# Optimization experiments

Hardware: AMD Instinct MI355X
Metric: run time of the kernel (lower is better)

## Reference

```python
import jax, jax.numpy as jnp
import numpy as np
from functools import partial

TAU = 2.0
BN_EPS = 1e-5
SG_ALPHA = 4.0  # spikingjelly surrogate.Sigmoid default

@jax.custom_vjp
def heaviside(x):
    return (x >= 0.0).astype(x.dtype)

def _heaviside_fwd(x):
    return heaviside(x), x

def _heaviside_bwd(x, g):
    s = jax.nn.sigmoid(SG_ALPHA * x)
    return (g * SG_ALPHA * s * (1.0 - s),)

heaviside.defvjp(_heaviside_fwd, _heaviside_bwd)

def lif(x_seq, v_threshold=1.0):
    # MultiStepLIFNode: tau=2, decay_input=True, v_reset=0 (hard reset), detach_reset
    def step(v, x):
        v = v + (x - v) / TAU
        s = heaviside(v - v_threshold)
        v = v * (1.0 - jax.lax.stop_gradient(s))
        return v, s
    _, s_seq = jax.lax.scan(step, jnp.zeros_like(x_seq[0]), x_seq)
    return s_seq

def conv1x1_bn(x, w, gamma, beta, mean, var, b=None):
    # x: [T,B,C,N]; w: [Cout,Cin]; 1x1 conv == channel matmul; BN in eval mode
    y = jnp.einsum('oc,tbcn->tbon', w, x)
    if b is not None:
        y = y + b[:, None]
    inv = gamma / jnp.sqrt(var + BN_EPS)
    return y * inv[:, None] + (beta - mean * inv)[:, None]

def setup_inputs() -> dict:
    key = jax.random.key(0)
    ks = jax.random.split(key, 24)
    T, B, C, N = 4, 32, 384, 196
    d = {}
    d['x'] = jax.random.normal(ks[0], (T, B, C, N), dtype=jnp.float32)
    d['policy'] = jax.random.uniform(ks[1], (T * B, N, 1), dtype=jnp.float32)
    scale = 1.0 / np.sqrt(C)
    for i, p in enumerate(['q', 'k', 'v', 'proj']):
        base = 2 + i * 5
        d[p + '_w'] = jax.random.normal(ks[base], (C, C), dtype=jnp.float32) * scale
        d[p + '_gamma'] = jnp.ones((C,), jnp.float32)
        d[p + '_beta'] = jnp.zeros((C,), jnp.float32)
        d[p + '_mean'] = jax.random.normal(ks[base + 1], (C,), dtype=jnp.float32) * 0.1
        d[p + '_var'] = jax.random.uniform(ks[base + 2], (C,), dtype=jnp.float32, minval=0.5, maxval=1.5)
    d['proj_b'] = jnp.zeros((C,), jnp.float32)
    return d

def _to_heads(s, H):
    T, B, C, N = s.shape
    # [T,B,C,N] -> [T,B,N,H,D] -> [T,B,H,N,D]
    return s.transpose(0, 1, 3, 2).reshape(T, B, N, H, C // H).transpose(0, 1, 3, 2, 4)

def reference(x, policy, q_w, q_gamma, q_beta, q_mean, q_var,
              k_w, k_gamma, k_beta, k_mean, k_var,
              v_w, v_gamma, v_beta, v_mean, v_var,
              proj_w, proj_gamma, proj_beta, proj_mean, proj_var, proj_b):
    T, B, C, N = x.shape
    H = 12
    attn_scale = 0.25
    q = _to_heads(lif(conv1x1_bn(x, q_w, q_gamma, q_beta, q_mean, q_var)), H)
    k = _to_heads(lif(conv1x1_bn(x, k_w, k_gamma, k_beta, k_mean, k_var)), H)
    v = _to_heads(lif(conv1x1_bn(x, v_w, v_gamma, v_beta, v_mean, v_var)), H)
    attn = jnp.einsum('tbhnd,tbhmd->tbhnm', q, k)
    # attention_policy: attn *= (policy + (1-policy)*eye)
    pol = policy.reshape(T, B, 1, 1, N)
    eye = jnp.eye(N, dtype=attn.dtype)
    attn = attn * (pol + (1.0 - pol) * eye)
    y = jnp.einsum('tbhnm,tbhmd->tbhnd', attn, v) * attn_scale
    y = y.transpose(0, 1, 2, 4, 3).reshape(T, B, C, N)
    y = lif(y, v_threshold=0.5)
    y = conv1x1_bn(y, proj_w, proj_gamma, proj_beta, proj_mean, proj_var, b=proj_b)
    return lif(y)
```

## Files before the change

kernel.cpp:

```cpp
#include <hip/hip_runtime.h>

typedef unsigned int u32;
typedef __bf16 bf16x8 __attribute__((ext_vector_type(8)));
typedef __bf16 bf16x4v __attribute__((ext_vector_type(4)));
typedef _Float16 f16x8 __attribute__((ext_vector_type(8)));
typedef float f32x4 __attribute__((ext_vector_type(4)));

#define Tn 4
#define Bn 32
#define Cn 384
#define Nn 196
#define Hn 12
#define CNn (Cn*Nn)
#define BCNn (Bn*CNn)
#define BHNn (Bn*Hn*Nn)
#define PBITS (Tn*BHNn)
#define TBCNn (Tn*BCNn)
#define NCOLS 6272
#define WSZ 147456

__device__ __forceinline__ void split3(float v, __bf16& h, __bf16& m, __bf16& l) {
  h = (__bf16)v;  float r = v - (float)h;
  m = (__bf16)r;  float r2 = r - (float)m;
  l = (__bf16)r2;
}
__device__ __forceinline__ void split2h(float v, _Float16& h, _Float16& l) {
  h = (_Float16)v;  l = (_Float16)(v - (float)h);
}

__device__ __forceinline__ void gl_lds16(const void* g, void* l) {
  __builtin_amdgcn_global_load_lds(
      (const __attribute__((address_space(1))) unsigned int*)g,
      (__attribute__((address_space(3))) unsigned int*)l, 16, 0, 0);
}

struct WSplitArgs {
  const float* w[4]; const float* g[4]; const float* be[4];
  const float* mu[4]; const float* va[4]; const float* bias;
};
__global__ __launch_bounds__(256) void prep(
    WSplitArgs a, _Float16* __restrict__ wsp16, __bf16* __restrict__ wspb,
    float* __restrict__ shv, const float* __restrict__ x,
    _Float16* __restrict__ xs) {
  __shared__ float tile[49 * 130];
  const int bx = blockIdx.x;
  const int tid = threadIdx.x;
  if (bx < 2304) {
    const int i = bx * 256 + tid;
    const int p = i / WSZ, r = i - p * WSZ;
    const int o = r / Cn, cc = r - o * Cn;
    const float iv = a.g[p][o] / sqrtf(a.va[p][o] + 1e-5f);
    const float wv = a.w[p][r] * iv;
    if (p < 3) {
      _Float16 h, l;
      split2h(wv, h, l);
      const int toff = ((o >> 4) * 12 + (cc >> 5)) * 512 +
                       (((cc >> 3) & 3) << 7) + ((o & 15) << 3) + (cc & 7);
      wsp16[(size_t)(p * 2 + 0) * WSZ + toff] = h;
      wsp16[(size_t)(p * 2 + 1) * WSZ + toff] = l;
    } else {
      __bf16 h, m, l;
      split3(wv, h, m, l);
      wspb[(size_t)0 * WSZ + r] = h;
      wspb[(size_t)1 * WSZ + r] = m;
      wspb[(size_t)2 * WSZ + r] = l;
    }
    if (cc == 0) {
      float sh = a.be[p][o] - a.mu[p][o] * iv;
      if (p == 3) sh += a.bias[o] * iv;
      shv[p * Cn + o] = sh;
    }
    return;
  }
  const int bid2 = bx - 2304;
  const int t = bid2 & 3, b = (bid2 >> 2) & 31, zz = bid2 >> 7;
  const int ct = zz >> 2, nch = zz & 3;
  const int c0 = ct * 128, n0 = nch * 49;
  for (int idx = tid; idx < 49 * 128; idx += 256) {
    const int n = idx % 49, c = idx / 49;
    tile[n * 130 + c] = x[(size_t)t * BCNn + (size_t)b * CNn +
                          (size_t)(c0 + c) * Nn + n0 + n];
  }
  __syncthreads();
  for (int idx = tid; idx < 49 * 64; idx += 256) {
    const int cp = idx & 63, n = idx >> 6;
    const float v0 = tile[n * 130 + cp * 2];
    const float v1 = tile[n * 130 + cp * 2 + 1];
    _Float16 h0, l0, h1, l1;
    split2h(v0, h0, l0);
    split2h(v1, h1, l1);
    const size_t col = (size_t)t * NCOLS + (size_t)b * Nn + n0 + n;
    union { _Float16 f[2]; u32 u; } uh, ul;
    uh.f[0] = h0; uh.f[1] = h1;
    ul.f[0] = l0; ul.f[1] = l1;
    ((u32*)(xs + col * Cn + c0))[cp] = uh.u;
    ((u32*)(xs + (size_t)TBCNn + col * Cn + c0))[cp] = ul.u;
  }
}

__global__ __launch_bounds__(256, 2) void gemm_qkv_lif(
    const _Float16* __restrict__ xs,
    const _Float16* __restrict__ wsp16,
    const float* __restrict__ shv,
    u32* __restrict__ bq, u32* __restrict__ bk, u32* __restrict__ bv)
{
  __shared__ _Float16 Bsw[3][2][64][32];
  const int orig = blockIdx.x;
  const int xcd = orig & 7, i8 = orig >> 3;
  const int wgid = xcd * 110 + (xcd < 2 ? xcd : 2) + i8;
  const int colt = wgid / 9, v = wgid - colt * 9;
  const int col0 = colt * 64;
  const int p = v / 3, mt = v - p * 3;
  const int o0 = mt * 128;
  const int tid = threadIdx.x, lane = tid & 63, wid = tid >> 6;
  const int wm = wid >> 1, wn = wid & 1;
  const int quad = lane >> 4, nl = lane & 15;
  u32* __restrict__ bits = (p == 0) ? bq : (p == 1) ? bk : bv;

  u32 afOff[2][4];
#pragma unroll
  for (int s = 0; s < 2; ++s)
#pragma unroll
    for (int mi = 0; mi < 4; ++mi)
      afOff[s][mi] = (u32)((((p * 2 + s) * WSZ) +
                            (mt * 8 + wm * 4 + mi) * 6144) * 2) +
                     (u32)(lane * 16);
  u32 bOff[2];
#pragma unroll
  for (int i = 0; i < 2; ++i) {
    const int c = i * 256 + wid * 64 + lane;
    const int s = c >> 8, rem = c & 255, row = rem >> 2, kb = rem & 3;
    const int kbs = kb ^ ((row >> 1) & 3);
    bOff[i] = (u32)(((size_t)s * TBCNn + (size_t)(col0 + row) * Cn + kbs * 8) * 2);
  }
  const char* wB = (const char*)wsp16;
  const char* xB = (const char*)xs;
  char* bD0 = (char*)&Bsw[0][0][0][0] + wid * 1024;

#define STAGE_B(g_) do {                                                   \
    const int t_ = ((g_) / 24) * 2 + ((g_) & 1);                           \
    const int kk_ = (((g_) % 24) >> 1);                                    \
    const u32 bk_ = (u32)(kk_ * 64) + (u32)t_ * (u32)(NCOLS * Cn * 2);     \
    char* d_ = bD0 + ((g_) % 3) * 8192;                                    \
    _Pragma("unroll") for (int i_ = 0; i_ < 2; ++i_)                       \
      gl_lds16(xB + bOff[i_] + bk_, d_ + i_ * 4096);                       \
  } while (0)
#define LOAD_AF(DST, g_) do {                                              \
    const u32 ak2_ = (u32)(((g_) % 12) * 1024);                            \
    _Pragma("unroll") for (int s_ = 0; s_ < 2; ++s_)                       \
    _Pragma("unroll") for (int m_ = 0; m_ < 4; ++m_)                       \
      DST[s_][m_] = *(const f16x8*)(wB + afOff[s_][m_] + ak2_);            \
  } while (0)

  f32x4 sh_[4];
#pragma unroll
  for (int mi = 0; mi < 4; ++mi)
    sh_[mi] = *(const f32x4*)&shv[p * Cn + o0 + wm * 64 + mi * 16 + quad * 4];

  f32x4 acc0[4][2], acc1[4][2];
  f32x4 vst[4][2] = {};
  f16x8 afA[2][4], afB[2][4];

  auto epi = [&](f32x4 (&ac)[4][2], int t) {
#pragma unroll
    for (int ni = 0; ni < 2; ++ni) {
      u32 w0 = 0, w1 = 0;
#pragma unroll
      for (int mi = 0; mi < 4; ++mi) {
#pragma unroll
        for (int r = 0; r < 4; ++r) {
          const float y = ac[mi][ni][r] + sh_[mi][r];
          const float vv = vst[mi][ni][r];
          const float nv = vv + (y - vv) * 0.5f;
          const bool sk = nv >= 1.0f;
          vst[mi][ni][r] = sk ? 0.f : nv;
          const u32 b1 = sk ? 1u : 0u;
          const int pos = ((mi & 1) << 4) + (quad << 2) + r;
          if (mi < 2) w0 |= b1 << pos; else w1 |= b1 << pos;
        }
      }
      w0 |= __shfl_xor(w0, 16); w0 |= __shfl_xor(w0, 32);
      w1 |= __shfl_xor(w1, 16); w1 |= __shfl_xor(w1, 32);
      if (quad == 0) {
        const int col = col0 + wn * 32 + ni * 16 + nl;
        const int bb = col / Nn, nn = col - bb * Nn;
        u32* bp = bits + (size_t)t * BHNn +
                  ((size_t)bb * Hn + (mt * 4 + wm * 2)) * Nn + nn;
        bp[0] = w0;
        bp[Nn] = w1;
      }
    }
  };

  auto sub = [&](f16x8 (&afc)[2][4], f16x8 (&afn)[2][4], int g) {
    const int kk = g % 12;
    const int be = (2 * g) % 3, bo = (2 * g + 1) % 3;
    if (g == 0)       asm volatile("s_waitcnt vmcnt(14)" ::: "memory");
    else if (g == 23) asm volatile("s_waitcnt vmcnt(18)" ::: "memory");
    else              asm volatile("s_waitcnt vmcnt(22)" ::: "memory");
    __builtin_amdgcn_s_barrier();
    __builtin_amdgcn_sched_barrier(0);
    if (g < 22) STAGE_B(2 * g + 4);
    __builtin_amdgcn_sched_barrier(0);
    if (kk == 0) {
#pragma unroll
      for (int mi = 0; mi < 4; ++mi)
#pragma unroll
        for (int ni = 0; ni < 2; ++ni) {
          acc0[mi][ni] = f32x4{0.f, 0.f, 0.f, 0.f};
          acc1[mi][ni] = f32x4{0.f, 0.f, 0.f, 0.f};
        }
    }
    {
      f16x8 bfr[2][2];
#pragma unroll
      for (int i = 0; i < 2; ++i) {
        const int rb = wn * 32 + i * 16 + nl;
        const int kb2 = (quad ^ ((rb >> 1) & 3)) * 8;
        bfr[0][i] = *(const f16x8*)&Bsw[be][0][rb][kb2];
        bfr[1][i] = *(const f16x8*)&Bsw[be][1][rb][kb2];
      }
      __builtin_amdgcn_s_setprio(1);
#pragma unroll
      for (int mi = 0; mi < 4; ++mi)
#pragma unroll
        for (int ni = 0; ni < 2; ++ni) {
          f32x4 c = acc0[mi][ni];
          c = __builtin_amdgcn_mfma_f32_16x16x32_f16(afc[0][mi], bfr[0][ni], c, 0, 0, 0);
          c = __builtin_amdgcn_mfma_f32_16x16x32_f16(afc[0][mi], bfr[1][ni], c, 0, 0, 0);
          c = __builtin_amdgcn_mfma_f32_16x16x32_f16(afc[1][mi], bfr[0][ni], c, 0, 0, 0);
          acc0[mi][ni] = c;
        }
      __builtin_amdgcn_s_setprio(0);
    }
    if (g == 22)      asm volatile("s_waitcnt vmcnt(12)" ::: "memory");
    else if (g == 23) asm volatile("s_waitcnt vmcnt(8)"  ::: "memory");
    else              asm volatile("s_waitcnt vmcnt(14)" ::: "memory");
    __builtin_amdgcn_s_barrier();
    __builtin_amdgcn_sched_barrier(0);
    if (g < 23) LOAD_AF(afn, g + 1);
    __builtin_amdgcn_sched_barrier(0);
    if (g < 22) STAGE_B(2 * g + 5);
    __builtin_amdgcn_sched_barrier(0);
    {
      f16x8 bfr[2][2];
#pragma unroll
      for (int i = 0; i < 2; ++i) {
        const int rb = wn * 32 + i * 16 + nl;
        const int kb2 = (quad ^ ((rb >> 1) & 3)) * 8;
        bfr[0][i] = *(const f16x8*)&Bsw[bo][0][rb][kb2];
        bfr[1][i] = *(const f16x8*)&Bsw[bo][1][rb][kb2];
      }
      __builtin_amdgcn_s_setprio(1);
#pragma unroll
      for (int mi = 0; mi < 4; ++mi)
#pragma unroll
        for (int ni = 0; ni < 2; ++ni) {
          f32x4 c = acc1[mi][ni];
          c = __builtin_amdgcn_mfma_f32_16x16x32_f16(afc[0][mi], bfr[0][ni], c, 0, 0, 0);
          c = __builtin_amdgcn_mfma_f32_16x16x32_f16(afc[0][mi], bfr[1][ni], c, 0, 0, 0);
          c = __builtin_amdgcn_mfma_f32_16x16x32_f16(afc[1][mi], bfr[0][ni], c, 0, 0, 0);
          acc1[mi][ni] = c;
        }
      __builtin_amdgcn_s_setprio(0);
    }
    if (kk == 11) {
      const int p2 = g / 12;
      epi(acc0, p2 * 2 + 0);
      epi(acc1, p2 * 2 + 1);
    }
  };

  STAGE_B(0); STAGE_B(1); STAGE_B(2);
  LOAD_AF(afA, 0);
  STAGE_B(3);

#pragma unroll 1
  for (int gp = 0; gp < 12; ++gp) {
    sub(afA, afB, 2 * gp);
    sub(afB, afA, 2 * gp + 1);
  }
#undef STAGE_B
#undef LOAD_AF
}

#define USTR 232
#define GSTR 40
__global__ __launch_bounds__(256, 2) void attn_lif(
    const u32* __restrict__ qb, const u32* __restrict__ kb,
    const u32* __restrict__ vb, const float* __restrict__ policy,
    __bf16* __restrict__ sp) {
  __shared__ u32 qs[208], ks[224], vs_[224];
  __shared__ float ps[224];
  __shared__ __bf16 psp[3][224];
  __shared__ __bf16 Ul[3][32][USTR];
  __shared__ __bf16 GT[3][32][GSTR];
  const int bh = blockIdx.x;
  const int bN = bh / Hn;
  const int h = bh - bN * Hn;
  const int tid = threadIdx.x;
  const int lane = tid & 63, wid = tid >> 6;
  const int quad = lane >> 4, nl = lane & 15;
  const int wm1 = wid >> 1, wn1 = wid & 1;
  const __bf16 one = (__bf16)1.0f, zero = (__bf16)0.0f;

  float vst[4][2][4] = {};

  for (int t = 0; t < Tn; ++t) {
    const int tb = t * Bn + bN;
    const int gid = tb * Hn + h;
    if (t) __syncthreads();
    for (int i = tid; i < 224; i += 256) {
      const bool in = i < Nn;
      if (i < 208) qs[i] = in ? qb[(size_t)gid * Nn + i] : 0u;
      ks[i] = in ? kb[(size_t)gid * Nn + i] : 0u;
      vs_[i] = in ? vb[(size_t)gid * Nn + i] : 0u;
      const float p = in ? policy[(size_t)tb * Nn + i] : 0.f;
      ps[i] = p;
      __bf16 hh, mm, ll;
      split3(p, hh, mm, ll);
      psp[0][i] = hh; psp[1][i] = mm; psp[2][i] = ll;
    }
    __syncthreads();

#pragma unroll
    for (int it = 0; it < 7; ++it) {
      const int idx = tid + it * 256;
      const int d = idx & 31, mg = idx >> 5;
      __bf16 u4[3][4];
#pragma unroll
      for (int j = 0; j < 4; ++j) {
        const int m = mg * 4 + j;
        const bool bit = (vs_[m] >> d) & 1u;
#pragma unroll
        for (int s = 0; s < 3; ++s)
          u4[s][j] = bit ? psp[s][m] : zero;
      }
#pragma unroll
      for (int s = 0; s < 3; ++s)
        *(bf16x4v*)&Ul[s][d][mg * 4] = *(bf16x4v*)u4[s];
    }
    __syncthreads();

    f32x4 gacc = {0.f, 0.f, 0.f, 0.f};
    const int crow = wm1 * 16 + nl;
    const int drow = wn1 * 16 + nl;
#pragma unroll
    for (int slab = 0; slab < 7; ++slab) {
      const int m0 = slab * 32 + quad * 8;
      u32 kw[8];
      *(uint4*)&kw[0] = *(const uint4*)&ks[m0];
      *(uint4*)&kw[4] = *(const uint4*)&ks[m0 + 4];
      __bf16 a8[8];
#pragma unroll
      for (int j = 0; j < 8; ++j)
        a8[j] = ((kw[j] >> crow) & 1u) ? one : zero;
      const bf16x8 af = *(const bf16x8*)a8;
#pragma unroll
      for (int s = 0; s < 3; ++s)
        gacc = __builtin_amdgcn_mfma_f32_16x16x32_bf16(
            af, *(const bf16x8*)&Ul[s][drow][slab * 32 + quad * 8], gacc, 0, 0, 0);
    }
#pragma unroll
    for (int r = 0; r < 4; ++r) {
      __bf16 gh, gm, gl;
      split3(gacc[r], gh, gm, gl);
      const int cc = wm1 * 16 + quad * 4 + r;
      GT[0][drow][cc] = gh;
      GT[1][drow][cc] = gm;
      GT[2][drow][cc] = gl;
    }
    __syncthreads();

    bf16x8 bfr2[3][2];
#pragma unroll
    for (int s = 0; s < 3; ++s)
#pragma unroll
      for (int nt = 0; nt < 2; ++nt)
        bfr2[s][nt] = *(const bf16x8*)&GT[s][nt * 16 + nl][quad * 8];

    f32x4 acc2[4][2] = {};
#pragma unroll
    for (int mi = 0; mi < 4; ++mi) {
      const int lt = wid + mi * 4;
      if (lt < 13) {
        const u32 qw = qs[lt * 16 + nl];
        __bf16 a8[8];
#pragma unroll
        for (int j = 0; j < 8; ++j)
          a8[j] = ((qw >> (quad * 8 + j)) & 1u) ? one : zero;
        const bf16x8 af2 = *(const bf16x8*)a8;
#pragma unroll
        for (int nt = 0; nt < 2; ++nt) {
          f32x4 c = acc2[mi][nt];
          c = __builtin_amdgcn_mfma_f32_16x16x32_bf16(af2, bfr2[0][nt], c, 0, 0, 0);
          c = __builtin_amdgcn_mfma_f32_16x16x32_bf16(af2, bfr2[1][nt], c, 0, 0, 0);
          c = __builtin_amdgcn_mfma_f32_16x16x32_bf16(af2, bfr2[2][nt], c, 0, 0, 0);
          acc2[mi][nt] = c;
        }
      }
    }
#pragma unroll
    for (int mi = 0; mi < 4; ++mi) {
      const int lt = wid + mi * 4;
      if (lt >= 13) continue;
#pragma unroll
      for (int r = 0; r < 4; ++r) {
        const int n = lt * 16 + quad * 4 + r;
        if (n >= Nn) continue;
        const float ann = (float)__popc(qs[n] & ks[n]);
        const float wd = ann * (1.0f - ps[n]);
        const u32 vn = vs_[n];
        __bf16* op = sp + (size_t)t * BCNn + ((size_t)bN * Nn + n) * Cn + h * 32;
#pragma unroll
        for (int nt = 0; nt < 2; ++nt) {
          const int d = nt * 16 + nl;
          const float bit = (float)((vn >> d) & 1u);
          const float y = (acc2[mi][nt][r] + wd * bit) * 0.25f;
          const float vv = vst[mi][nt][r];
          const float nv = vv + (y - vv) * 0.5f;
          const bool s = nv >= 0.5f;
          vst[mi][nt][r] = s ? 0.f : nv;
          op[d] = (__bf16)(s ? 1.0f : 0.0f);
        }
      }
    }
  }
}

__global__ __launch_bounds__(256, 3) void gemm_proj_lif(
    const __bf16* __restrict__ sp, const __bf16* __restrict__ wspb,
    const float* __restrict__ shv, float* __restrict__ out)
{
  __shared__ __bf16 Asw[3][3][64][32];
  __shared__ __bf16 Bsw[3][64][32];
  const int orig = blockIdx.x;
  const int xcd = orig & 7, i8 = orig >> 3;
  const int wgid = xcd * 73 + (xcd < 4 ? xcd : 4) + i8;
  const int colt = wgid / 6, ot = wgid - colt * 6;
  const int col0 = colt * 64;
  const int o0 = ot * 64;
  const int tid = threadIdx.x, lane = tid & 63, wid = tid >> 6;
  const int wm = wid >> 1, wn = wid & 1;
  const int quad = lane >> 4, nl = lane & 15;

  u32 aOff[3], bOff;
#pragma unroll
  for (int i = 0; i < 3; ++i) {
    const int c = i * 256 + wid * 64 + lane;
    const int s = c >> 8, rem = c & 255, row = rem >> 2, kb = rem & 3;
    const int kbs = kb ^ ((row >> 1) & 3);
    aOff[i] = (u32)(((s * WSZ) + (o0 + row) * Cn + kbs * 8) * 2);
  }
  {
    const int c = wid * 64 + lane;
    const int row = c >> 2, kb = c & 3;
    const int kbs = kb ^ ((row >> 1) & 3);
    bOff = (u32)(((size_t)(col0 + row) * Cn + kbs * 8) * 2);
  }
  const char* wB = (const char*)wspb;
  const char* sB = (const char*)sp;
  char* aD0 = (char*)&Asw[0][0][0][0] + wid * 1024;
  char* bD0 = (char*)&Bsw[0][0][0] + wid * 1024;

#define STAGE_A(ai_) do {                                                  \
    const u32 ak_ = (u32)(((ai_) % 12) * 64);                              \
    char* d_ = aD0 + ((ai_) % 3) * 12288;                                  \
    _Pragma("unroll") for (int i_ = 0; i_ < 3; ++i_)                       \
      gl_lds16(wB + aOff[i_] + ak_, d_ + i_ * 4096);                       \
  } while (0)
#define STAGE_B(g_) do {                                                   \
    const int t_ = ((g_) / 24) * 2 + ((g_) & 1);                           \
    const int kk_ = (((g_) % 24) >> 1);                                    \
    const u32 bk_ = (u32)(kk_ * 64) + (u32)t_ * (u32)(BCNn * 2);           \
    gl_lds16(sB + bOff + bk_, bD0 + ((g_) % 3) * 4096);                    \
  } while (0)

  f32x4 sh_[2];
#pragma unroll
  for (int mi = 0; mi < 2; ++mi)
    sh_[mi] = *(const f32x4*)&shv[3 * Cn + o0 + wm * 32 + mi * 16 + quad * 4];

  f32x4 acc0[2][2], acc1[2][2];
  f32x4 vst[2][2] = {};

  auto epi = [&](f32x4 (&ac)[2][2], int t) {
#pragma unroll
    for (int mi = 0; mi < 2; ++mi) {
      const int ob = o0 + wm * 32 + mi * 16 + quad * 4;
#pragma unroll
      for (int ni = 0; ni < 2; ++ni) {
        const int col = col0 + wn * 32 + ni * 16 + nl;
        const int bb = col / Nn, nn = col - bb * Nn;
        float* op = out + (size_t)t * BCNn + (size_t)bb * CNn + nn;
#pragma unroll
        for (int r = 0; r < 4; ++r) {
          const float y = ac[mi][ni][r] + sh_[mi][r];
          const float vv = vst[mi][ni][r];
          const float nv = vv + (y - vv) * 0.5f;
          const bool sk = nv >= 1.0f;
          vst[mi][ni][r] = sk ? 0.f : nv;
          op[(size_t)(ob + r) * Nn] = sk ? 1.0f : 0.0f;
        }
      }
    }
  };

  STAGE_B(0); STAGE_A(0); STAGE_B(1); STAGE_A(1);

#pragma unroll 1
  for (int gg = 0; gg < 24; ++gg) {
    const int abuf = gg % 3;
    const int be = (2 * gg) % 3, bo = (2 * gg + 1) % 3;
    const int kk = gg % 12;

    if (gg < 23) { asm volatile("s_waitcnt vmcnt(4)" ::: "memory"); }
    else         { asm volatile("s_waitcnt vmcnt(1)" ::: "memory"); }
    __builtin_amdgcn_s_barrier();
    __builtin_amdgcn_sched_barrier(0);
    if (gg < 23) STAGE_B(2 * gg + 2);
    if (kk == 0) {
#pragma unroll
      for (int mi = 0; mi < 2; ++mi)
#pragma unroll
        for (int ni = 0; ni < 2; ++ni) {
          acc0[mi][ni] = f32x4{0.f, 0.f, 0.f, 0.f};
          acc1[mi][ni] = f32x4{0.f, 0.f, 0.f, 0.f};
        }
    }
    bf16x8 af[3][2];
#pragma unroll
    for (int mi = 0; mi < 2; ++mi) {
      const int ra = wm * 32 + mi * 16 + nl;
      const int ka = (quad ^ ((ra >> 1) & 3)) * 8;
#pragma unroll
      for (int s = 0; s < 3; ++s)
        af[s][mi] = *(const bf16x8*)&Asw[abuf][s][ra][ka];
    }
    {
      bf16x8 bfr[2];
#pragma unroll
      for (int ni = 0; ni < 2; ++ni) {
        const int rb = wn * 32 + ni * 16 + nl;
        const int kb2 = (quad ^ ((rb >> 1) & 3)) * 8;
        bfr[ni] = *(const bf16x8*)&Bsw[be][rb][kb2];
      }
      __builtin_amdgcn_s_setprio(1);
#pragma unroll
      for (int mi = 0; mi < 2; ++mi)
#pragma unroll
        for (int ni = 0; ni < 2; ++ni) {
          f32x4 c = acc0[mi][ni];
          c = __builtin_amdgcn_mfma_f32_16x16x32_bf16(af[0][mi], bfr[ni], c, 0, 0, 0);
          c = __builtin_amdgcn_mfma_f32_16x16x32_bf16(af[1][mi], bfr[ni], c, 0, 0, 0);
          c = __builtin_amdgcn_mfma_f32_16x16x32_bf16(af[2][mi], bfr[ni], c, 0, 0, 0);
          acc0[mi][ni] = c;
        }
      __builtin_amdgcn_s_setprio(0);
    }

    if (gg < 23) { asm volatile("s_waitcnt vmcnt(4)" ::: "memory"); }
    else         { asm volatile("s_waitcnt vmcnt(0)" ::: "memory"); }
    __builtin_amdgcn_s_barrier();
    __builtin_amdgcn_sched_barrier(0);
    if (gg < 23) STAGE_B(2 * gg + 3);
    if (gg < 22) STAGE_A(gg + 2);
    {
      bf16x8 bfr[2];
#pragma unroll
      for (int ni = 0; ni < 2; ++ni) {
        const int rb = wn * 32 + ni * 16 + nl;
        const int kb2 = (quad ^ ((rb >> 1) & 3)) * 8;
        bfr[ni] = *(const bf16x8*)&Bsw[bo][rb][kb2];
      }
      __builtin_amdgcn_s_setprio(1);
#pragma unroll
      for (int mi = 0; mi < 2; ++mi)
#pragma unroll
        for (int ni = 0; ni < 2; ++ni) {
          f32x4 c = acc1[mi][ni];
          c = __builtin_amdgcn_mfma_f32_16x16x32_bf16(af[0][mi], bfr[ni], c, 0, 0, 0);
          c = __builtin_amdgcn_mfma_f32_16x16x32_bf16(af[1][mi], bfr[ni], c, 0, 0, 0);
          c = __builtin_amdgcn_mfma_f32_16x16x32_bf16(af[2][mi], bfr[ni], c, 0, 0, 0);
          acc1[mi][ni] = c;
        }
      __builtin_amdgcn_s_setprio(0);
    }
    if (kk == 11) {
      const int p2 = gg / 12;
      epi(acc0, p2 * 2 + 0);
      epi(acc1, p2 * 2 + 1);
    }
  }
#undef STAGE_A
#undef STAGE_B
}

extern "C" void kernel_launch(void* const* d_in, const int* in_sizes, int n_in,
                              void* d_out, int out_size, void* d_ws, size_t ws_size,
                              hipStream_t stream) {
  const float* x      = (const float*)d_in[0];
  const float* policy = (const float*)d_in[1];
  const float* qw = (const float*)d_in[2];
  const float* qg = (const float*)d_in[3];
  const float* qb_ = (const float*)d_in[4];
  const float* qm = (const float*)d_in[5];
  const float* qv = (const float*)d_in[6];
  const float* kw = (const float*)d_in[7];
  const float* kg = (const float*)d_in[8];
  const float* kbe = (const float*)d_in[9];
  const float* km = (const float*)d_in[10];
  const float* kv = (const float*)d_in[11];
  const float* vw = (const float*)d_in[12];
  const float* vg = (const float*)d_in[13];
  const float* vbe = (const float*)d_in[14];
  const float* vm = (const float*)d_in[15];
  const float* vv = (const float*)d_in[16];
  const float* pw = (const float*)d_in[17];
  const float* pg = (const float*)d_in[18];
  const float* pbe = (const float*)d_in[19];
  const float* pm = (const float*)d_in[20];
  const float* pv = (const float*)d_in[21];
  const float* pbias = (const float*)d_in[22];
  float* out = (float*)d_out;

  char* base = (char*)d_ws;
  _Float16* xs   = (_Float16*)base;
  _Float16* wsp16 = (_Float16*)(base + (size_t)TBCNn * 4);
  __bf16* wspb   = (__bf16*)((char*)wsp16 + (size_t)6 * WSZ * 2);
  float* shv     = (float*)((char*)wspb + (size_t)3 * WSZ * 2);
  u32* bq        = (u32*)((char*)shv + 4 * Cn * 4);
  u32* bk = bq + PBITS;
  u32* bv = bk + PBITS;
  __bf16* sp     = (__bf16*)(bv + PBITS);

  WSplitArgs wa;
  wa.w[0] = qw; wa.g[0] = qg; wa.be[0] = qb_; wa.mu[0] = qm; wa.va[0] = qv;
  wa.w[1] = kw; wa.g[1] = kg; wa.be[1] = kbe; wa.mu[1] = km; wa.va[1] = kv;
  wa.w[2] = vw; wa.g[2] = vg; wa.be[2] = vbe; wa.mu[2] = vm; wa.va[2] = vv;
  wa.w[3] = pw; wa.g[3] = pg; wa.be[3] = pbe; wa.mu[3] = pm; wa.va[3] = pv;
  wa.bias = pbias;
  prep<<<3840, 256, 0, stream>>>(wa, wsp16, wspb, shv, x, xs);

  gemm_qkv_lif<<<882, 256, 0, stream>>>(xs, wsp16, shv, bq, bk, bv);
  attn_lif<<<Bn * Hn, 256, 0, stream>>>(bq, bk, bv, policy, sp);
  gemm_proj_lif<<<588, 256, 0, stream>>>(sp, wspb, shv, out);
}
```

Before: 276.6 us.

## Load proj weights directly into registers from tiled layout and deepen B pipeline

```diff
diff --git a/kernel.cpp b/kernel.cpp
--- a/kernel.cpp
+++ b/kernel.cpp
@@ -51,19 +51,19 @@
     const int o = r / Cn, cc = r - o * Cn;
     const float iv = a.g[p][o] / sqrtf(a.va[p][o] + 1e-5f);
     const float wv = a.w[p][r] * iv;
+    const int toff = ((o >> 4) * 12 + (cc >> 5)) * 512 +
+                     (((cc >> 3) & 3) << 7) + ((o & 15) << 3) + (cc & 7);
     if (p < 3) {
       _Float16 h, l;
       split2h(wv, h, l);
-      const int toff = ((o >> 4) * 12 + (cc >> 5)) * 512 +
-                       (((cc >> 3) & 3) << 7) + ((o & 15) << 3) + (cc & 7);
       wsp16[(size_t)(p * 2 + 0) * WSZ + toff] = h;
       wsp16[(size_t)(p * 2 + 1) * WSZ + toff] = l;
     } else {
       __bf16 h, m, l;
       split3(wv, h, m, l);
-      wspb[(size_t)0 * WSZ + r] = h;
-      wspb[(size_t)1 * WSZ + r] = m;
-      wspb[(size_t)2 * WSZ + r] = l;
+      wspb[(size_t)0 * WSZ + toff] = h;
+      wspb[(size_t)1 * WSZ + toff] = m;
+      wspb[(size_t)2 * WSZ + toff] = l;
     }
     if (cc == 0) {
       float sh = a.be[p][o] - a.mu[p][o] * iv;
@@ -104,7 +104,7 @@
     const float* __restrict__ shv,
     u32* __restrict__ bq, u32* __restrict__ bk, u32* __restrict__ bv)
 {
-  __shared__ _Float16 Bsw[3][2][64][32];
+  __shared__ _Float16 Bsw[5][2][64][32];
   const int orig = blockIdx.x;
   const int xcd = orig & 7, i8 = orig >> 3;
   const int wgid = xcd * 110 + (xcd < 2 ? xcd : 2) + i8;
@@ -141,7 +141,7 @@
     const int t_ = ((g_) / 24) * 2 + ((g_) & 1);                           \
     const int kk_ = (((g_) % 24) >> 1);                                    \
     const u32 bk_ = (u32)(kk_ * 64) + (u32)t_ * (u32)(NCOLS * Cn * 2);     \
-    char* d_ = bD0 + ((g_) % 3) * 8192;                                    \
+    char* d_ = bD0 + ((g_) % 5) * 8192;                                    \
     _Pragma("unroll") for (int i_ = 0; i_ < 2; ++i_)                       \
       gl_lds16(xB + bOff[i_] + bk_, d_ + i_ * 4096);                       \
   } while (0)
@@ -194,7 +194,7 @@
 
   auto sub = [&](f16x8 (&afc)[2][4], f16x8 (&afn)[2][4], int g) {
     const int kk = g % 12;
-    const int be = (2 * g) % 3, bo = (2 * g + 1) % 3;
+    const int be = (2 * g) % 5, bo = (2 * g + 1) % 5;
     if (g == 0)       asm volatile("s_waitcnt vmcnt(14)" ::: "memory");
     else if (g == 23) asm volatile("s_waitcnt vmcnt(18)" ::: "memory");
     else              asm volatile("s_waitcnt vmcnt(22)" ::: "memory");
@@ -432,8 +432,7 @@
     const __bf16* __restrict__ sp, const __bf16* __restrict__ wspb,
     const float* __restrict__ shv, float* __restrict__ out)
 {
-  __shared__ __bf16 Asw[3][3][64][32];
-  __shared__ __bf16 Bsw[3][64][32];
+  __shared__ __bf16 Bsw[5][64][32];
   const int orig = blockIdx.x;
   const int xcd = orig & 7, i8 = orig >> 3;
   const int wgid = xcd * 73 + (xcd < 4 ? xcd : 4) + i8;
@@ -444,14 +443,14 @@
   const int wm = wid >> 1, wn = wid & 1;
   const int quad = lane >> 4, nl = lane & 15;
 
-  u32 aOff[3], bOff;
-#pragma unroll
-  for (int i = 0; i < 3; ++i) {
-    const int c = i * 256 + wid * 64 + lane;
-    const int s = c >> 8, rem = c & 255, row = rem >> 2, kb = rem & 3;
-    const int kbs = kb ^ ((row >> 1) & 3);
-    aOff[i] = (u32)(((s * WSZ) + (o0 + row) * Cn + kbs * 8) * 2);
-  }
+  u32 afOff[3][2];
+#pragma unroll
+  for (int s = 0; s < 3; ++s)
+#pragma unroll
+    for (int mi = 0; mi < 2; ++mi)
+      afOff[s][mi] = (u32)(((s * WSZ) + (ot * 4 + wm * 2 + mi) * 6144) * 2) +
+                     (u32)(lane * 16);
+  u32 bOff;
   {
     const int c = wid * 64 + lane;
     const int row = c >> 2, kb = c & 3;
@@ -460,20 +459,19 @@
   }
   const char* wB = (const char*)wspb;
   const char* sB = (const char*)sp;
-  char* aD0 = (char*)&Asw[0][0][0][0] + wid * 1024;
   char* bD0 = (char*)&Bsw[0][0][0] + wid * 1024;
 
-#define STAGE_A(ai_) do {                                                  \
-    const u32 ak_ = (u32)(((ai_) % 12) * 64);                              \
-    char* d_ = aD0 + ((ai_) % 3) * 12288;                                  \
-    _Pragma("unroll") for (int i_ = 0; i_ < 3; ++i_)                       \
-      gl_lds16(wB + aOff[i_] + ak_, d_ + i_ * 4096);                       \
-  } while (0)
 #define STAGE_B(g_) do {                                                   \
     const int t_ = ((g_) / 24) * 2 + ((g_) & 1);                           \
     const int kk_ = (((g_) % 24) >> 1);                                    \
     const u32 bk_ = (u32)(kk_ * 64) + (u32)t_ * (u32)(BCNn * 2);           \
-    gl_lds16(sB + bOff + bk_, bD0 + ((g_) % 3) * 4096);                    \
+    gl_lds16(sB + bOff + bk_, bD0 + ((g_) % 5) * 4096);                    \
+  } while (0)
+#define LOAD_AF(DST, g_) do {                                              \
+    const u32 ak2_ = (u32)(((g_) % 12) * 1024);                            \
+    _Pragma("unroll") for (int s_ = 0; s_ < 3; ++s_)                       \
+    _Pragma("unroll") for (int m_ = 0; m_ < 2; ++m_)                       \
+      DST[s_][m_] = *(const bf16x8*)(wB + afOff[s_][m_] + ak2_);           \
   } while (0)
 
   f32x4 sh_[2];
@@ -483,6 +481,7 @@
 
   f32x4 acc0[2][2], acc1[2][2];
   f32x4 vst[2][2] = {};
+  bf16x8 afA[3][2], afB[3][2];
 
   auto epi = [&](f32x4 (&ac)[2][2], int t) {
 #pragma unroll
@@ -506,19 +505,15 @@
     }
   };
 
-  STAGE_B(0); STAGE_A(0); STAGE_B(1); STAGE_A(1);
-
-#pragma unroll 1
-  for (int gg = 0; gg < 24; ++gg) {
-    const int abuf = gg % 3;
-    const int be = (2 * gg) % 3, bo = (2 * gg + 1) % 3;
-    const int kk = gg % 12;
-
-    if (gg < 23) { asm volatile("s_waitcnt vmcnt(4)" ::: "memory"); }
-    else         { asm volatile("s_waitcnt vmcnt(1)" ::: "memory"); }
+  auto sub = [&](bf16x8 (&afc)[3][2], bf16x8 (&afn)[3][2], int g) {
+    const int kk = g % 12;
+    const int be = (2 * g) % 5, bo = (2 * g + 1) % 5;
+    if (g == 23) asm volatile("s_waitcnt vmcnt(0)" ::: "memory");
+    else         asm volatile("s_waitcnt vmcnt(1)" ::: "memory");
     __builtin_amdgcn_s_barrier();
     __builtin_amdgcn_sched_barrier(0);
-    if (gg < 23) STAGE_B(2 * gg + 2);
+    if (g < 22) STAGE_B(2 * g + 4);
+    __builtin_amdgcn_sched_barrier(0);
     if (kk == 0) {
 #pragma unroll
       for (int mi = 0; mi < 2; ++mi)
@@ -527,15 +522,6 @@
           acc0[mi][ni] = f32x4{0.f, 0.f, 0.f, 0.f};
           acc1[mi][ni] = f32x4{0.f, 0.f, 0.f, 0.f};
         }
-    }
-    bf16x8 af[3][2];
-#pragma unroll
-    for (int mi = 0; mi < 2; ++mi) {
-      const int ra = wm * 32 + mi * 16 + nl;
-      const int ka = (quad ^ ((ra >> 1) & 3)) * 8;
-#pragma unroll
-      for (int s = 0; s < 3; ++s)
-        af[s][mi] = *(const bf16x8*)&Asw[abuf][s][ra][ka];
     }
     {
       bf16x8 bfr[2];
@@ -551,20 +537,22 @@
 #pragma unroll
         for (int ni = 0; ni < 2; ++ni) {
           f32x4 c = acc0[mi][ni];
-          c = __builtin_amdgcn_mfma_f32_16x16x32_bf16(af[0][mi], bfr[ni], c, 0, 0, 0);
-          c = __builtin_amdgcn_mfma_f32_16x16x32_bf16(af[1][mi], bfr[ni], c, 0, 0, 0);
-          c = __builtin_amdgcn_mfma_f32_16x16x32_bf16(af[2][mi], bfr[ni], c, 0, 0, 0);
+          c = __builtin_amdgcn_mfma_f32_16x16x32_bf16(afc[0][mi], bfr[ni], c, 0, 0, 0);
+          c = __builtin_amdgcn_mfma_f32_16x16x32_bf16(afc[1][mi], bfr[ni], c, 0, 0, 0);
+          c = __builtin_amdgcn_mfma_f32_16x16x32_bf16(afc[2][mi], bfr[ni], c, 0, 0, 0);
           acc0[mi][ni] = c;
         }
       __builtin_amdgcn_s_setprio(0);
     }
-
-    if (gg < 23) { asm volatile("s_waitcnt vmcnt(4)" ::: "memory"); }
-    else         { asm volatile("s_waitcnt vmcnt(0)" ::: "memory"); }
+    if (g == 22)      asm volatile("s_waitcnt vmcnt(1)" ::: "memory");
+    else if (g == 23) asm volatile("s_waitcnt vmcnt(0)" ::: "memory");
+    else              asm volatile("s_waitcnt vmcnt(2)" ::: "memory");
     __builtin_amdgcn_s_barrier();
     __builtin_amdgcn_sched_barrier(0);
-    if (gg < 23) STAGE_B(2 * gg + 3);
-    if (gg < 22) STAGE_A(gg + 2);
+    if (g < 23) LOAD_AF(afn, g + 1);
+    __builtin_amdgcn_sched_barrier(0);
+    if (g < 22) STAGE_B(2 * g + 5);
+    __builtin_amdgcn_sched_barrier(0);
     {
       bf16x8 bfr[2];
 #pragma unroll
@@ -579,21 +567,31 @@
 #pragma unroll
         for (int ni = 0; ni < 2; ++ni) {
           f32x4 c = acc1[mi][ni];
-          c = __builtin_amdgcn_mfma_f32_16x16x32_bf16(af[0][mi], bfr[ni], c, 0, 0, 0);
-          c = __builtin_amdgcn_mfma_f32_16x16x32_bf16(af[1][mi], bfr[ni], c, 0, 0, 0);
-          c = __builtin_amdgcn_mfma_f32_16x16x32_bf16(af[2][mi], bfr[ni], c, 0, 0, 0);
+          c = __builtin_amdgcn_mfma_f32_16x16x32_bf16(afc[0][mi], bfr[ni], c, 0, 0, 0);
+          c = __builtin_amdgcn_mfma_f32_16x16x32_bf16(afc[1][mi], bfr[ni], c, 0, 0, 0);
+          c = __builtin_amdgcn_mfma_f32_16x16x32_bf16(afc[2][mi], bfr[ni], c, 0, 0, 0);
           acc1[mi][ni] = c;
         }
       __builtin_amdgcn_s_setprio(0);
     }
     if (kk == 11) {
-      const int p2 = gg / 12;
+      const int p2 = g / 12;
       epi(acc0, p2 * 2 + 0);
       epi(acc1, p2 * 2 + 1);
     }
-  }
-#undef STAGE_A
+  };
+
+  STAGE_B(0); STAGE_B(1); STAGE_B(2);
+  LOAD_AF(afA, 0);
+  STAGE_B(3);
+
+#pragma unroll 1
+  for (int gp = 0; gp < 12; ++gp) {
+    sub(afA, afB, 2 * gp);
+    sub(afB, afA, 2 * gp + 1);
+  }
 #undef STAGE_B
+#undef LOAD_AF
 }
 
 extern "C" void kernel_launch(void* const* d_in, const int* in_sizes, int n_in,
```

Result: no change. 274.1 us, median of 2 (-0.9%).
